# Kernel optimization log

Measured on AMD Instinct MI355X. Metric: run time of the kernel, lower is better.

## Reference

```python
import jax, jax.numpy as jnp
import numpy as np

NEG_SLOPE = 0.2  # PyG GATConv default leaky_relu slope
BN_EPS = 1e-5


def gat_conv(x_src, x_dst, src, dst, w_src, w_dst, att_src, att_dst, bias):
    """Bipartite PyG GATConv, heads=H, concat=False (mean over heads), add_self_loops=True.
    x_src: [Ns, F], x_dst: [Nd, F]; src/dst: [E] int edge index; w_*: [F, H*C]; att_*: [H, C]; bias: [C].
    """
    H, C = att_src.shape
    n_dst = x_dst.shape[0]
    hs = (x_src @ w_src).reshape(-1, H, C)            # [Ns, H, C]
    hd = (x_dst @ w_dst).reshape(-1, H, C)            # [Nd, H, C]
    a_s = (hs * att_src[None]).sum(-1)                # [Ns, H]
    a_d = (hd * att_dst[None]).sum(-1)                # [Nd, H]
    # PyG adds self loops with num_nodes = min(Ns, Nd) for bipartite inputs
    n_loop = min(x_src.shape[0], n_dst)
    loop = jnp.arange(n_loop, dtype=src.dtype)
    src = jnp.concatenate([src, loop])
    dst = jnp.concatenate([dst, loop])
    e = jax.nn.leaky_relu(a_s[src] + a_d[dst], NEG_SLOPE)           # [E+L, H]
    m = jax.ops.segment_max(e, dst, num_segments=n_dst)             # [Nd, H]
    ex = jnp.exp(e - m[dst])
    den = jax.ops.segment_sum(ex, dst, num_segments=n_dst)
    alpha = ex / (den[dst] + 1e-16)                                 # neighborhood softmax
    msg = hs[src] * alpha[:, :, None]                               # [E+L, H, C]
    out = jax.ops.segment_sum(msg, dst, num_segments=n_dst)         # [Nd, H, C]
    return out.mean(axis=1) + bias


def _forward(user_ids, ingredient_ids, recipe_x, ing_src, ing_dst, ub_src, ub_dst,
             user_table, ing_table, W_rl, b_rl, bn_gamma, bn_beta,
             g1_ws, g1_wd, g1_as, g1_ad, g1_b,
             g2_ws, g2_wd, g2_as, g2_ad, g2_b):
    # nn.Embedding(max_norm=1.0): renorm looked-up rows to L2 norm <= 1
    u = user_table[user_ids]
    un = jnp.linalg.norm(u, axis=-1, keepdims=True)
    u = u * jnp.where(un > 1.0, 1.0 / (un + 1e-7), 1.0)
    # static ingredient embedding lookup
    ing = ing_table[ingredient_ids]
    # recipe linear + BatchNorm (training-mode batch stats; dropout off = eval)
    r = recipe_x @ W_rl + b_rl
    mu = r.mean(axis=0)
    var = ((r - mu) ** 2).mean(axis=0)
    r = bn_gamma * (r - mu) * jax.lax.rsqrt(var + BN_EPS) + bn_beta
    # ingredient -> recipe GAT, residual add
    r = r + gat_conv(ing, r, ing_src, ing_dst, g1_ws, g1_wd, g1_as, g1_ad, g1_b)
    # user -> recipe GAT
    r = gat_conv(u, r, ub_src, ub_dst, g2_ws, g2_wd, g2_as, g2_ad, g2_b)
    return r


def setup_inputs() -> dict:
    key = jax.random.key(0)
    ks = jax.random.split(key, 24)
    NU, NR, NI = 50000, 100000, 20000
    D_IN, H, C = 20, 2, 128
    E1, E2 = 400000, 800000
    s = 0.05
    f32 = jnp.float32
    inp = {
        "user_ids": jax.random.randint(ks[0], (NU,), 0, NU, dtype=jnp.int32),
        "ingredient_ids": jax.random.randint(ks[1], (NI,), 0, NI, dtype=jnp.int32),
        "recipe_x": jax.random.normal(ks[2], (NR, D_IN), f32),
        "ing_src": jax.random.randint(ks[3], (E1,), 0, NI, dtype=jnp.int32),
        "ing_dst": jax.random.randint(ks[4], (E1,), 0, NR, dtype=jnp.int32),
        "ub_src": jax.random.randint(ks[5], (E2,), 0, NU, dtype=jnp.int32),
        "ub_dst": jax.random.randint(ks[6], (E2,), 0, NR, dtype=jnp.int32),
        "user_table": jax.random.normal(ks[7], (NU, C), f32) * s,
        "ing_table": jax.random.normal(ks[8], (NI, C), f32) * s,
        "W_rl": jax.random.normal(ks[9], (D_IN, C), f32) * s,
        "b_rl": jnp.zeros((C,), f32),
        "bn_gamma": jnp.ones((C,), f32),
        "bn_beta": jnp.zeros((C,), f32),
        "g1_ws": jax.random.normal(ks[10], (C, H * C), f32) * s,
        "g1_wd": jax.random.normal(ks[11], (C, H * C), f32) * s,
        "g1_as": jax.random.normal(ks[12], (H, C), f32) * s,
        "g1_ad": jax.random.normal(ks[13], (H, C), f32) * s,
        "g1_b": jnp.zeros((C,), f32),
        "g2_ws": jax.random.normal(ks[14], (C, H * C), f32) * s,
        "g2_wd": jax.random.normal(ks[15], (C, H * C), f32) * s,
        "g2_as": jax.random.normal(ks[16], (H, C), f32) * s,
        "g2_ad": jax.random.normal(ks[17], (H, C), f32) * s,
        "g2_b": jnp.zeros((C,), f32),
    }
    return inp


def reference(user_ids, ingredient_ids, recipe_x, ing_src, ing_dst, ub_src, ub_dst,
              user_table, ing_table, W_rl, b_rl, bn_gamma, bn_beta,
              g1_ws, g1_wd, g1_as, g1_ad, g1_b,
              g2_ws, g2_wd, g2_as, g2_ad, g2_b):
    return _forward(user_ids, ingredient_ids, recipe_x, ing_src, ing_dst, ub_src, ub_dst,
                    user_table, ing_table, W_rl, b_rl, bn_gamma, bn_beta,
                    g1_ws, g1_wd, g1_as, g1_ad, g1_b,
                    g2_ws, g2_wd, g2_as, g2_ad, g2_b)
```

## Files before the change

### kernel.cpp

```cpp
#include <hip/hip_runtime.h>
#include <hip/hip_bf16.h>
#include <math.h>

#define DIN 20
#define C 128
#define HC 256
#define EB1 8192
#define EB2 2048
#define MAXNB 400

typedef unsigned short u16;
typedef unsigned int u32;
typedef unsigned long long u64;
typedef __bf16 bf16x8 __attribute__((ext_vector_type(8)));
typedef float f32x4 __attribute__((ext_vector_type(4)));

__device__ __forceinline__ float bfbits2f(unsigned int lo16) {
    return __uint_as_float(lo16 << 16);
}
__device__ __forceinline__ u16 f2bf_rne(float f) {
    unsigned int b = __float_as_uint(f);
    return (u16)((b + 0x7FFFu + ((b >> 16) & 1u)) >> 16);
}

__device__ __forceinline__ void scan512f(u32* cnt, u32* off, u32* wsum4) {
    int t = threadIdx.x;
    int l = t & 63, w = t >> 6;
    u32 a = cnt[2 * t], b = cnt[2 * t + 1];
    u32 s = a + b;
    u32 isc = s;
    #pragma unroll
    for (int o = 1; o < 64; o <<= 1) {
        u32 n = __shfl_up(isc, o);
        if (l >= o) isc += n;
    }
    if (l == 63) wsum4[w] = isc;
    __syncthreads();
    u32 pre = 0;
    if (w > 0) pre += wsum4[0];
    if (w > 1) pre += wsum4[1];
    if (w > 2) pre += wsum4[2];
    u32 excl = pre + isc - s;
    off[2 * t] = excl;
    off[2 * t + 1] = excl + a;
    __syncthreads();
}

__device__ __forceinline__ void edge_at(int i, const int* s1, const int* d1,
    const int* s2, const int* d2, int E1, int T1, int E2, int NR,
    int& s, int& key)
{
    if (i < T1) {
        if (i < E1) { s = s1[i]; key = d1[i]; }
        else        { s = i - E1; key = i - E1; }
    } else {
        int k = i - T1;
        if (k < E2) { s = s2[k]; key = NR + d2[k]; }
        else        { s = k - E2; key = NR + (k - E2); }
    }
}

__global__ __launch_bounds__(256) void k_init(const float* __restrict__ x, int NR,
    float* __restrict__ stats, int SB,
    const int* __restrict__ src1, const int* __restrict__ dst1,
    const int* __restrict__ src2, const int* __restrict__ dst2,
    int E1, int L1, int E2, int L2, int NB, u32* __restrict__ bucketCnt)
{
    __shared__ float L[256][DIN];
    __shared__ u32 cnt[MAXNB];
    int t = threadIdx.x;
    if (blockIdx.x < SB) {
        int r = blockIdx.x * 256 + t;
        if (r < NR) {
            #pragma unroll
            for (int k = 0; k < DIN; k++) L[t][k] = x[r * DIN + k];
        } else {
            #pragma unroll
            for (int k = 0; k < DIN; k++) L[t][k] = 0.f;
        }
        __syncthreads();
        if (t < 210) {
            int p = 0, q = t;
            while (q >= DIN - p) { q -= (DIN - p); p++; }
            q += p;
            float acc = 0.f;
            for (int rr = 0; rr < 256; rr++) acc += L[rr][p] * L[rr][q];
            atomicAdd(&stats[p * DIN + q], acc);
            if (p != q) atomicAdd(&stats[q * DIN + p], acc);
        } else if (t < 230) {
            int k = t - 210;
            float acc = 0.f;
            for (int rr = 0; rr < 256; rr++) acc += L[rr][k];
            atomicAdd(&stats[400 + k], acc);
        }
        return;
    }
    for (int i = t; i < NB; i += 256) cnt[i] = 0;
    __syncthreads();
    int T1 = E1 + L1, T = T1 + E2 + L2;
    int base = (blockIdx.x - SB) * EB1;
    int nE = T - base; if (nE > EB1) nE = EB1;
    for (int j = t; j < nE; j += 256) {
        int s, key;
        edge_at(base + j, src1, dst1, src2, dst2, E1, T1, E2, NR, s, key);
        atomicAdd(&cnt[key >> 9], 1u);
    }
    __syncthreads();
    for (int b = t; b < NB; b += 256) {
        u32 c = cnt[b];
        if (c) atomicAdd(&bucketCnt[b], c);
    }
}

__global__ __launch_bounds__(256) void k_precomp_pack(float* __restrict__ stats,
    const float* __restrict__ W,
    const float* __restrict__ gamma, const float* __restrict__ beta,
    const float* __restrict__ g1_wd, const float* __restrict__ g1_ad,
    const float* __restrict__ g2_wd, const float* __restrict__ g2_ad,
    const float* __restrict__ g1_ws, const float* __restrict__ g1_as,
    const float* __restrict__ g2_ws, const float* __restrict__ g2_as,
    const float* __restrict__ g1b, float invN, u16* __restrict__ wsp,
    const u32* __restrict__ bucketCnt, int NB, int n2,
    u32* __restrict__ bucketBase, u32* __restrict__ gcur, int* __restrict__ off)
{
    int t = threadIdx.x;
    if (blockIdx.x == 33) {
        __shared__ u32 cnt[512], offL[512], wsum4[4];
        for (int i = t; i < 512; i += 256) cnt[i] = (i < NB) ? bucketCnt[i] : 0u;
        __syncthreads();
        scan512f(cnt, offL, wsum4);
        for (int i = t; i < NB; i += 256) {
            u32 v = offL[i];
            bucketBase[i] = v;
            gcur[i] = v;
        }
        if (t == 0) {
            u32 total = offL[511] + cnt[511];
            bucketBase[NB] = total;
            off[n2] = (int)total;
        }
        return;
    }
    if (blockIdx.x > 0) {
        int idx0 = ((blockIdx.x - 1) * 256 + t) * 4;
        #pragma unroll
        for (int i = 0; i < 4; i++) {
            int flat = idx0 + i;
            int j = flat & 7;
            int lane = (flat >> 3) & 63;
            int kb = (flat >> 9) & 3;
            int nt = flat >> 11;
            int k = kb * 32 + (lane >> 4) * 8 + j;
            int n = nt * 16 + (lane & 15);
            wsp[flat] = f2bf_rne(g2_ws[k * HC + n]);
        }
        return;
    }
    __shared__ float Sm[420];
    __shared__ float Wm[DIN * C];
    __shared__ float vd1s[256];
    __shared__ float vd2s[256];
    __shared__ float sS[128];
    __shared__ float sSh[128];
    for (int i = t; i < 420; i += 256) Sm[i] = stats[i];
    for (int i = t; i < DIN * C; i += 256) Wm[i] = W[i];
    __syncthreads();
    if (t < C) {
        float w[DIN];
        #pragma unroll
        for (int k = 0; k < DIN; k++) w[k] = Wm[k * C + t];
        float mb = 0.f;
        #pragma unroll
        for (int k = 0; k < DIN; k++) mb += Sm[400 + k] * invN * w[k];
        float e2 = 0.f;
        for (int p = 0; p < DIN; p++) {
            float acc2 = 0.f;
            #pragma unroll
            for (int q = 0; q < DIN; q++) acc2 += Sm[p * DIN + q] * w[q];
            e2 += w[p] * acc2;
        }
        e2 *= invN;
        float var = e2 - mb * mb;
        float s = gamma[t] * rsqrtf(var + 1e-5f);
        float sh = beta[t] - s * mb;
        stats[420 + t] = s;
        stats[548 + t] = sh;
        sS[t] = s;
        sSh[t] = sh;
    }
    {
        int k = t >> 1, h = t & 1;
        const float4* wd1 = (const float4*)(g1_wd + k * HC + h * C);
        const float4* wd2 = (const float4*)(g2_wd + k * HC + h * C);
        const float4* ws1 = (const float4*)(g1_ws + k * HC + h * C);
        const float4* ws2 = (const float4*)(g2_ws + k * HC + h * C);
        const float4* ad1 = (const float4*)(g1_ad + h * C);
        const float4* ad2 = (const float4*)(g2_ad + h * C);
        const float4* as1 = (const float4*)(g1_as + h * C);
        const float4* as2 = (const float4*)(g2_as + h * C);
        float a1 = 0.f, a2 = 0.f, s1 = 0.f, s2 = 0.f;
        #pragma unroll 4
        for (int q = 0; q < 32; q++) {
            float4 x, y;
            x = wd1[q]; y = ad1[q];
            a1 += x.x * y.x + x.y * y.y + x.z * y.z + x.w * y.w;
            x = wd2[q]; y = ad2[q];
            a2 += x.x * y.x + x.y * y.y + x.z * y.z + x.w * y.w;
            x = ws1[q]; y = as1[q];
            s1 += x.x * y.x + x.y * y.y + x.z * y.z + x.w * y.w;
            x = ws2[q]; y = as2[q];
            s2 += x.x * y.x + x.y * y.y + x.z * y.z + x.w * y.w;
        }
        stats[676 + t] = a1;
        stats[932 + t] = a2;
        stats[1200 + t] = s1;
        stats[1456 + t] = s2;
        vd1s[t] = a1;
        vd2s[t] = a2;
    }
    __syncthreads();
    {
        int k = t >> 1, h = t & 1;
        const float4* ws1p = (const float4*)(g1_ws + k * HC + h * C);
        float t0 = 0.f, t1 = 0.f;
        #pragma unroll 4
        for (int q = 0; q < 32; q++) {
            float4 wv = ws1p[q];
            int c = q * 4;
            t0 += wv.x * vd2s[(c + 0) * 2 + 0] + wv.y * vd2s[(c + 1) * 2 + 0]
                + wv.z * vd2s[(c + 2) * 2 + 0] + wv.w * vd2s[(c + 3) * 2 + 0];
            t1 += wv.x * vd2s[(c + 0) * 2 + 1] + wv.y * vd2s[(c + 1) * 2 + 1]
                + wv.z * vd2s[(c + 2) * 2 + 1] + wv.w * vd2s[(c + 3) * 2 + 1];
        }
        stats[1712 + t * 2 + 0] = t0;
        stats[1712 + t * 2 + 1] = t1;
    }
    if (t < 2) {
        float cb = 0.f;
        for (int k = 0; k < C; k++) cb += g1b[k] * vd2s[k * 2 + t];
        stats[1188 + t] = cb;
    }
    if (t < 80) {
        int k = t >> 2, h4 = t & 3, h = h4 & 1;
        const float* vs = (h4 < 2) ? vd1s : vd2s;
        float acc = 0.f;
        for (int c = 0; c < C; c++) acc += sS[c] * Wm[k * C + c] * vs[c * 2 + h];
        stats[2240 + t] = acc;
    } else if (t < 84) {
        int h4 = t - 80, h = h4 & 1;
        const float* vs = (h4 < 2) ? vd1s : vd2s;
        float acc = 0.f;
        for (int c = 0; c < C; c++) acc += sSh[c] * vs[c * 2 + h];
        stats[2320 + h4] = acc;
    }
}

__global__ __launch_bounds__(256) void k_feat(
    const float* __restrict__ x, int NR, int R0B, int IB,
    const float* __restrict__ ing_table, const int* __restrict__ ing_ids, int NI,
    const float* __restrict__ user_table, const int* __restrict__ user_ids, int NU,
    const u16* __restrict__ wsp, const float* __restrict__ stats,
    float* __restrict__ a_d, float* __restrict__ advd,
    float* __restrict__ a_si, float* __restrict__ psi,
    u16* __restrict__ hs16, float* __restrict__ a_su)
{
    __shared__ float fv[84];
    __shared__ float u1s[256];
    __shared__ float Ts[512];
    __shared__ __align__(16) u16 A[32 * 136];
    __shared__ float u2s[256];
    int t = threadIdx.x;
    int bid = blockIdx.x;
    if (bid < R0B) {
        if (t < 84) fv[t] = stats[2240 + t];
        __syncthreads();
        int r = bid * 256 + t;
        if (r < NR) {
            const float4* xp = (const float4*)(x + (size_t)r * DIN);
            float4 v0 = xp[0], v1 = xp[1], v2 = xp[2], v3 = xp[3], v4 = xp[4];
            float xv[20] = {v0.x, v0.y, v0.z, v0.w, v1.x, v1.y, v1.z, v1.w,
                            v2.x, v2.y, v2.z, v2.w, v3.x, v3.y, v3.z, v3.w,
                            v4.x, v4.y, v4.z, v4.w};
            float a0 = 0.f, a1 = 0.f, b0 = 0.f, b1 = 0.f;
            #pragma unroll
            for (int k = 0; k < DIN; k++) {
                float xvk = xv[k];
                a0 += xvk * fv[k * 4 + 0];
                a1 += xvk * fv[k * 4 + 1];
                b0 += xvk * fv[k * 4 + 2];
                b1 += xvk * fv[k * 4 + 3];
            }
            ((float2*)a_d)[r]  = make_float2(a0 + fv[80], a1 + fv[81]);
            ((float2*)advd)[r] = make_float2(b0 + fv[82], b1 + fv[83]);
        }
        return;
    }
    if (bid < R0B + IB) {
        u1s[t] = stats[1200 + t];
        Ts[t] = stats[1712 + t];
        Ts[256 + t] = stats[1968 + t];
        __syncthreads();
        int r = t >> 3, cg = t & 7;
        int row = (bid - R0B) * 32 + r;
        float as0 = 0.f, as1 = 0.f, p00 = 0.f, p01 = 0.f, p10 = 0.f, p11 = 0.f;
        if (row < NI) {
            const float* xp = ing_table + (size_t)ing_ids[row] * C + cg * 16;
            #pragma unroll
            for (int q = 0; q < 4; q++) {
                float4 v = ((const float4*)xp)[q];
                float xvv[4] = {v.x, v.y, v.z, v.w};
                #pragma unroll
                for (int jj = 0; jj < 4; jj++) {
                    int k = cg * 16 + q * 4 + jj;
                    float xx = xvv[jj];
                    as0 += xx * u1s[k * 2 + 0];
                    as1 += xx * u1s[k * 2 + 1];
                    p00 += xx * Ts[k * 4 + 0];
                    p01 += xx * Ts[k * 4 + 1];
                    p10 += xx * Ts[k * 4 + 2];
                    p11 += xx * Ts[k * 4 + 3];
                }
            }
        }
        #pragma unroll
        for (int m = 1; m <= 4; m <<= 1) {
            as0 += __shfl_xor(as0, m); as1 += __shfl_xor(as1, m);
            p00 += __shfl_xor(p00, m); p01 += __shfl_xor(p01, m);
            p10 += __shfl_xor(p10, m); p11 += __shfl_xor(p11, m);
        }
        if (cg == 0 && row < NI) {
            ((float2*)a_si)[row] = make_float2(as0, as1);
            float4 pv; pv.x = p00; pv.y = p01; pv.z = p10; pv.w = p11;
            ((float4*)psi)[row] = pv;
        }
        return;
    }
    u2s[t] = stats[1456 + t];
    int rowBase = (bid - R0B - IB) * 32;
    int r = t >> 3, cg = t & 7;
    int row = rowBase + r;
    float xv[16];
    if (row < NU) {
        const float* xp = user_table + (size_t)user_ids[row] * C + cg * 16;
        #pragma unroll
        for (int q = 0; q < 4; q++) {
            float4 v = ((const float4*)xp)[q];
            xv[q * 4 + 0] = v.x; xv[q * 4 + 1] = v.y;
            xv[q * 4 + 2] = v.z; xv[q * 4 + 3] = v.w;
        }
    } else {
        #pragma unroll
        for (int q = 0; q < 16; q++) xv[q] = 0.f;
    }
    float ss = 0.f;
    #pragma unroll
    for (int q = 0; q < 16; q++) ss += xv[q] * xv[q];
    #pragma unroll
    for (int m = 1; m <= 4; m <<= 1) ss += __shfl_xor(ss, m);
    float nn = sqrtf(ss);
    float f = (nn > 1.f) ? 1.f / (nn + 1e-7f) : 1.f;
    float as0 = 0.f, as1 = 0.f;
    #pragma unroll
    for (int q = 0; q < 16; q++) {
        xv[q] *= f;
        int k = cg * 16 + q;
        as0 += xv[q] * u2s[k * 2 + 0];
        as1 += xv[q] * u2s[k * 2 + 1];
    }
    #pragma unroll
    for (int m = 1; m <= 4; m <<= 1) {
        as0 += __shfl_xor(as0, m); as1 += __shfl_xor(as1, m);
    }
    if (cg == 0 && row < NU) ((float2*)a_su)[row] = make_float2(as0, as1);
    {
        union { u16 h[16]; uint4 u4[2]; } pk;
        #pragma unroll
        for (int q = 0; q < 16; q++) pk.h[q] = f2bf_rne(xv[q]);
        uint4* dst = (uint4*)&A[r * 136 + cg * 16];
        dst[0] = pk.u4[0];
        dst[1] = pk.u4[1];
    }
    __syncthreads();
    int w = t >> 6, l = t & 63;
    int m15 = l & 15, q4 = l >> 4;
    bf16x8 afrag[2][4];
    #pragma unroll
    for (int mt = 0; mt < 2; mt++)
        #pragma unroll
        for (int kb = 0; kb < 4; kb++)
            afrag[mt][kb] = *(const bf16x8*)&A[(mt * 16 + m15) * 136 + kb * 32 + q4 * 8];
    f32x4 acc[2][4];
    #pragma unroll
    for (int mt = 0; mt < 2; mt++)
        #pragma unroll
        for (int i = 0; i < 4; i++) acc[mt][i] = (f32x4){0.f, 0.f, 0.f, 0.f};
    #pragma unroll
    for (int kb = 0; kb < 4; kb++) {
        #pragma unroll
        for (int i = 0; i < 4; i++) {
            int nt = w * 4 + i;
            bf16x8 bfrag = *(const bf16x8*)&wsp[((nt * 4 + kb) * 64 + l) * 8];
            acc[0][i] = __builtin_amdgcn_mfma_f32_16x16x32_bf16(afrag[0][kb], bfrag, acc[0][i], 0, 0, 0);
            acc[1][i] = __builtin_amdgcn_mfma_f32_16x16x32_bf16(afrag[1][kb], bfrag, acc[1][i], 0, 0, 0);
        }
    }
    #pragma unroll
    for (int mt = 0; mt < 2; mt++) {
        #pragma unroll
        for (int i = 0; i < 4; i++) {
            int col = (w * 4 + i) * 16 + m15;
            #pragma unroll
            for (int rr = 0; rr < 4; rr++) {
                int rw = rowBase + mt * 16 + q4 * 4 + rr;
                if (rw < NU) hs16[(size_t)rw * HC + col] = f2bf_rne(acc[mt][i][rr]);
            }
        }
    }
}

__global__ __launch_bounds__(256) void kA2(const int* __restrict__ src1, const int* __restrict__ dst1,
    const int* __restrict__ src2, const int* __restrict__ dst2,
    int E1, int L1, int E2, int L2, int NR, int NB,
    u32* __restrict__ gcur, u64* __restrict__ pairs)
{
    __shared__ u64 ldsE[EB2];
    __shared__ u64 ldsS[EB2];
    __shared__ u32 cntA[512], cntB[512], offL[512], wsum4[4];
    __shared__ u32 gbase[MAXNB];
    int t = threadIdx.x;
    for (int i = t; i < 512; i += 256) { cntA[i] = 0; cntB[i] = 0; }
    __syncthreads();
    int T1 = E1 + L1, T = T1 + E2 + L2;
    int base = blockIdx.x * EB2;
    int nE = T - base; if (nE > EB2) nE = EB2;
    for (int j = t; j < nE; j += 256) {
        int s, key;
        edge_at(base + j, src1, dst1, src2, dst2, E1, T1, E2, NR, s, key);
        ldsE[j] = ((u64)(u32)key << 32) | (u32)s;
        atomicAdd(&cntA[key >> 9], 1u);
    }
    __syncthreads();
    scan512f(cntA, offL, wsum4);
    for (int b = t; b < NB; b += 256) {
        u32 c = cntA[b];
        gbase[b] = c ? atomicAdd(&gcur[b], c) : 0u;
    }
    __syncthreads();
    for (int j = t; j < nE; j += 256) {
        u64 e = ldsE[j];
        u32 b = ((u32)(e >> 32)) >> 9;
        u32 r = atomicAdd(&cntB[b], 1u);
        ldsS[offL[b] + r] = e;
    }
    __syncthreads();
    for (int j = t; j < nE; j += 256) {
        u64 e = ldsS[j];
        u32 b = ((u32)(e >> 32)) >> 9;
        pairs[gbase[b] + ((u32)j - offL[b])] = e;
    }
}

__global__ __launch_bounds__(256) void kB(const u64* __restrict__ pairs,
    const u32* __restrict__ bucketBase, int n2,
    int* __restrict__ off, int* __restrict__ sorted)
{
    __shared__ u32 cntA[512], cntB[512], offL[512], wsum4[4];
    __shared__ u32 ldsS[8192];
    int b = blockIdx.x;
    int t = threadIdx.x;
    u32 beg = bucketBase[b], end = bucketBase[b + 1];
    int dstBase = b << 9;
    for (int i = t; i < 512; i += 256) { cntA[i] = 0; cntB[i] = 0; }
    __syncthreads();
    for (u32 j = beg + t; j < end; j += 256) {
        u32 key = (u32)(pairs[j] >> 32);
        atomicAdd(&cntA[key - dstBase], 1u);
    }
    __syncthreads();
    scan512f(cntA, offL, wsum4);
    for (int d = t; d < 512; d += 256) {
        int gk = dstBase + d;
        if (gk < n2) off[gk] = (int)(beg + offL[d]);
    }
    u32 cnt = end - beg;
    bool fast = cnt <= 8192u;
    __syncthreads();
    for (u32 j = beg + t; j < end; j += 256) {
        u64 e = pairs[j];
        u32 d = (u32)(e >> 32) - dstBase;
        u32 r = atomicAdd(&cntB[d], 1u);
        u32 pos = offL[d] + r;
        if (fast) ldsS[pos] = (u32)e;
        else sorted[beg + pos] = (int)(u32)e;
    }
    __syncthreads();
    if (fast) {
        for (u32 j = t; j < cnt; j += 256) sorted[beg + j] = (int)ldsS[j];
    }
}

__global__ __launch_bounds__(256) void k_agg(const int* __restrict__ off, const int* __restrict__ sorted,
    const float* __restrict__ a_si, const float* __restrict__ psi,
    const float* __restrict__ a_d1, const float* __restrict__ advd,
    const float* __restrict__ cb,
    const float* __restrict__ a_su, const u16* __restrict__ hs16,
    const float* __restrict__ bias, int NR, float* __restrict__ out)
{
    int wave = threadIdx.x >> 6, lane = threadIdx.x & 63;
    int d = blockIdx.x * 4 + wave;
    if (d >= NR) return;
    int beg = off[d], end = off[d + 1];
    float ad0 = a_d1[d * 2 + 0], ad1 = a_d1[d * 2 + 1];
    float w0s = 0.f, w1s = 0.f, a00 = 0.f, a01 = 0.f, a10 = 0.f, a11 = 0.f;
    for (int j = beg + lane; j < end; j += 64) {
        int s = sorted[j];
        float2 as = ((const float2*)a_si)[s];
        float e0 = as.x + ad0; e0 = (e0 >= 0.f) ? e0 : 0.2f * e0;
        float e1 = as.y + ad1; e1 = (e1 >= 0.f) ? e1 : 0.2f * e1;
        float x0 = __expf(e0), x1 = __expf(e1);
        float4 p = ((const float4*)psi)[s];
        w0s += x0; w1s += x1;
        a00 += x0 * p.x; a01 += x0 * p.y;
        a10 += x1 * p.z; a11 += x1 * p.w;
    }
    #pragma unroll
    for (int o = 1; o < 64; o <<= 1) {
        w0s += __shfl_xor(w0s, o); w1s += __shfl_xor(w1s, o);
        a00 += __shfl_xor(a00, o); a01 += __shfl_xor(a01, o);
        a10 += __shfl_xor(a10, o); a11 += __shfl_xor(a11, o);
    }
    float inv0g = 1.f / (w0s + 1e-16f), inv1g = 1.f / (w1s + 1e-16f);
    float r0 = advd[d * 2 + 0] + cb[0] + 0.5f * (a00 * inv0g + a10 * inv1g);
    float r1 = advd[d * 2 + 1] + cb[1] + 0.5f * (a01 * inv0g + a11 * inv1g);
    int beg2 = off[NR + d], end2 = off[NR + d + 1];
    int head = lane >> 5;
    int q = lane & 31;
    u32 laneoff = (u32)(head * 256 + q * 8);
    int hsel = lane & 32;
    float adh = head ? r1 : r0;
    float wsum = 0.f;
    float acc0 = 0.f, acc1 = 0.f, acc2 = 0.f, acc3 = 0.f;
    const char* hbase = (const char*)hs16;

    for (int base = beg2; base < end2; base += 32) {
        int rem = end2 - base; if (rem > 32) rem = 32;
        int j = q; if (j >= rem) j = rem - 1;
        int sp = sorted[base + j];
        u32 boff = ((u32)sp) << 9;
        float asv = a_su[sp * 2 + head];
        float ee = asv + adh; ee = (ee >= 0.f) ? ee : 0.2f * ee;
        float wcomb = __expf(ee);
        int e = 0;
        for (; e + 4 <= rem; e += 4) {
            u32 b0 = __shfl(boff, e + 0), b1 = __shfl(boff, e + 1);
            u32 b2 = __shfl(boff, e + 2), b3 = __shfl(boff, e + 3);
            uint2 g0 = *(const uint2*)(hbase + (b0 + laneoff));
            uint2 g1 = *(const uint2*)(hbase + (b1 + laneoff));
            uint2 g2 = *(const uint2*)(hbase + (b2 + laneoff));
            uint2 g3 = *(const uint2*)(hbase + (b3 + laneoff));
            float W0 = __shfl(wcomb, hsel + e + 0);
            float W1 = __shfl(wcomb, hsel + e + 1);
            float W2 = __shfl(wcomb, hsel + e + 2);
            float W3 = __shfl(wcomb, hsel + e + 3);
            wsum += (W0 + W1) + (W2 + W3);
            acc0 += W0 * bfbits2f(g0.x & 0xFFFFu);
            acc1 += W0 * __uint_as_float(g0.x & 0xFFFF0000u);
            acc2 += W0 * bfbits2f(g0.y & 0xFFFFu);
            acc3 += W0 * __uint_as_float(g0.y & 0xFFFF0000u);
            acc0 += W1 * bfbits2f(g1.x & 0xFFFFu);
            acc1 += W1 * __uint_as_float(g1.x & 0xFFFF0000u);
            acc2 += W1 * bfbits2f(g1.y & 0xFFFFu);
            acc3 += W1 * __uint_as_float(g1.y & 0xFFFF0000u);
            acc0 += W2 * bfbits2f(g2.x & 0xFFFFu);
            acc1 += W2 * __uint_as_float(g2.x & 0xFFFF0000u);
            acc2 += W2 * bfbits2f(g2.y & 0xFFFFu);
            acc3 += W2 * __uint_as_float(g2.y & 0xFFFF0000u);
            acc0 += W3 * bfbits2f(g3.x & 0xFFFFu);
            acc1 += W3 * __uint_as_float(g3.x & 0xFFFF0000u);
            acc2 += W3 * bfbits2f(g3.y & 0xFFFFu);
            acc3 += W3 * __uint_as_float(g3.y & 0xFFFF0000u);
        }
        for (; e < rem; e++) {
            u32 b0 = __shfl(boff, e);
            float W = __shfl(wcomb, hsel + e);
            uint2 g = *(const uint2*)(hbase + (b0 + laneoff));
            wsum += W;
            acc0 += W * bfbits2f(g.x & 0xFFFFu);
            acc1 += W * __uint_as_float(g.x & 0xFFFF0000u);
            acc2 += W * bfbits2f(g.y & 0xFFFFu);
            acc3 += W * __uint_as_float(g.y & 0xFFFF0000u);
        }
    }
    float inv = 1.f / (wsum + 1e-16f);
    float v0 = acc0 * inv, v1 = acc1 * inv, v2 = acc2 * inv, v3 = acc3 * inv;
    v0 = 0.5f * (v0 + __shfl_xor(v0, 32));
    v1 = 0.5f * (v1 + __shfl_xor(v1, 32));
    v2 = 0.5f * (v2 + __shfl_xor(v2, 32));
    v3 = 0.5f * (v3 + __shfl_xor(v3, 32));
    if (lane < 32) {
        float4 bb = ((const float4*)bias)[q];
        float4 o;
        o.x = v0 + bb.x; o.y = v1 + bb.y; o.z = v2 + bb.z; o.w = v3 + bb.w;
        ((float4*)(out + (size_t)d * C))[q] = o;
    }
}

extern "C" void kernel_launch(void* const* d_in, const int* in_sizes, int n_in,
                              void* d_out, int out_size, void* d_ws, size_t ws_size,
                              hipStream_t stream) {
    const int*   user_ids       = (const int*)d_in[0];
    const int*   ingredient_ids = (const int*)d_in[1];
    const float* recipe_x       = (const float*)d_in[2];
    const int*   ing_src        = (const int*)d_in[3];
    const int*   ing_dst        = (const int*)d_in[4];
    const int*   ub_src         = (const int*)d_in[5];
    const int*   ub_dst         = (const int*)d_in[6];
    const float* user_table     = (const float*)d_in[7];
    const float* ing_table      = (const float*)d_in[8];
    const float* W_rl           = (const float*)d_in[9];
    const float* bn_gamma       = (const float*)d_in[11];
    const float* bn_beta        = (const float*)d_in[12];
    const float* g1_ws          = (const float*)d_in[13];
    const float* g1_wd          = (const float*)d_in[14];
    const float* g1_as          = (const float*)d_in[15];
    const float* g1_ad          = (const float*)d_in[16];
    const float* g1_b           = (const float*)d_in[17];
    const float* g2_ws          = (const float*)d_in[18];
    const float* g2_wd          = (const float*)d_in[19];
    const float* g2_as          = (const float*)d_in[20];
    const float* g2_ad          = (const float*)d_in[21];
    const float* g2_b           = (const float*)d_in[22];

    int NU = in_sizes[0];
    int NI = in_sizes[1];
    int NR = in_sizes[2] / DIN;
    int E1 = in_sizes[3];
    int E2 = in_sizes[5];
    int Nmax = (NI > NU) ? NI : NU;
    int L1 = (NI < NR) ? NI : NR;
    int L2 = (NU < NR) ? NU : NR;
    int Etot = E1 + L1 + E2 + L2;
    int n2 = 2 * NR;
    int NB = (n2 + 511) >> 9;

    char* w = (char*)d_ws;
    u16*   hs16  = (u16*)w;    w += (size_t)Nmax * HC * 2;
    float* a_si  = (float*)w;  w += (size_t)NI * 2 * 4;
    float* a_su  = (float*)w;  w += (size_t)NU * 2 * 4;
    float* psi   = (float*)w;  w += (size_t)NI * 4 * 4;
    float* a_d   = (float*)w;  w += (size_t)NR * 2 * 4;
    float* advd  = (float*)w;  w += (size_t)NR * 2 * 4;
    float* stats = (float*)w;  w += 2432 * 4;
    u32*   bucketCnt  = (u32*)w; w += MAXNB * 4;
    u16*   wsp   = (u16*)w;    w += 32768 * 2;
    u32*   bucketBase = (u32*)w; w += (MAXNB + 1) * 4;
    u32*   gcur  = (u32*)w;    w += MAXNB * 4;
    int*   off   = (int*)w;    w += (size_t)(n2 + 1) * 4;
    int*   sorted= (int*)w;    w += (size_t)Etot * 4;
    w = (char*)(((size_t)w + 15) & ~(size_t)15);
    u64*   pairs = (u64*)w;    w += (size_t)Etot * 8;

    hipMemsetAsync(stats, 0, (2432 + MAXNB) * 4, stream);

    int SB = (NR + 255) / 256;
    int AB = (Etot + EB1 - 1) / EB1;
    k_init<<<SB + AB, 256, 0, stream>>>(recipe_x, NR, stats, SB,
                                        ing_src, ing_dst, ub_src, ub_dst,
                                        E1, L1, E2, L2, NB, bucketCnt);
    k_precomp_pack<<<34, 256, 0, stream>>>(stats, W_rl, bn_gamma, bn_beta,
                                           g1_wd, g1_ad, g2_wd, g2_ad,
                                           g1_ws, g1_as, g2_ws, g2_as, g1_b,
                                           1.0f / NR, wsp,
                                           bucketCnt, NB, n2, bucketBase, gcur, off);
    kA2<<<(Etot + EB2 - 1) / EB2, 256, 0, stream>>>(ing_src, ing_dst, ub_src, ub_dst,
                                                    E1, L1, E2, L2, NR, NB, gcur, pairs);
    int R0B = (NR + 255) / 256;
    int IB  = (NI + 31) / 32;
    int HB  = (NU + 31) / 32;
    k_feat<<<R0B + IB + HB, 256, 0, stream>>>(recipe_x, NR, R0B, IB,
                                              ing_table, ingredient_ids, NI,
                                              user_table, user_ids, NU,
                                              wsp, stats, a_d, advd, a_si, psi,
                                              hs16, a_su);
    kB<<<NB, 256, 0, stream>>>(pairs, bucketBase, n2, off, sorted);
    k_agg<<<(NR + 3) / 4, 256, 0, stream>>>(off, sorted, a_si, psi, a_d, advd,
                                            stats + 1188, a_su, hs16, g2_b, NR,
                                            (float*)d_out);
}
```

Before: 352.4 us.

## Replace two-pass bucket sort with per-destination counting sort fused into feature kernel

Edge grouping by destination now uses a counting sort: global atomic histogram per destination key, a block-level scan with a tiny second-level prefix, and an atomic scatter of source ids. The scatter runs as extra blocks inside the feature kernel, which removes the kA2 and kB kernels and the 64-bit pairs buffer. The user-aggregation loop also now processes two edges per wave step with 16-byte gathers per lane. The cost is heavy global atomic contention on hot destinations and a non-deterministic order of edges within each segment.

Result: slower. 456.6 us (+29.6%).

```diff
diff --git a/kernel.cpp b/kernel.cpp
--- a/kernel.cpp
+++ b/kernel.cpp
@@ -6,8 +6,7 @@
 #define C 128
 #define HC 256
 #define EB1 8192
-#define EB2 2048
-#define MAXNB 400
+#define EBS 4096
 
 typedef unsigned short u16;
 typedef unsigned int u32;
@@ -23,51 +22,12 @@
     return (u16)((b + 0x7FFFu + ((b >> 16) & 1u)) >> 16);
 }
 
-__device__ __forceinline__ void scan512f(u32* cnt, u32* off, u32* wsum4) {
-    int t = threadIdx.x;
-    int l = t & 63, w = t >> 6;
-    u32 a = cnt[2 * t], b = cnt[2 * t + 1];
-    u32 s = a + b;
-    u32 isc = s;
-    #pragma unroll
-    for (int o = 1; o < 64; o <<= 1) {
-        u32 n = __shfl_up(isc, o);
-        if (l >= o) isc += n;
-    }
-    if (l == 63) wsum4[w] = isc;
-    __syncthreads();
-    u32 pre = 0;
-    if (w > 0) pre += wsum4[0];
-    if (w > 1) pre += wsum4[1];
-    if (w > 2) pre += wsum4[2];
-    u32 excl = pre + isc - s;
-    off[2 * t] = excl;
-    off[2 * t + 1] = excl + a;
-    __syncthreads();
-}
-
-__device__ __forceinline__ void edge_at(int i, const int* s1, const int* d1,
-    const int* s2, const int* d2, int E1, int T1, int E2, int NR,
-    int& s, int& key)
-{
-    if (i < T1) {
-        if (i < E1) { s = s1[i]; key = d1[i]; }
-        else        { s = i - E1; key = i - E1; }
-    } else {
-        int k = i - T1;
-        if (k < E2) { s = s2[k]; key = NR + d2[k]; }
-        else        { s = k - E2; key = NR + (k - E2); }
-    }
-}
-
 __global__ __launch_bounds__(256) void k_init(const float* __restrict__ x, int NR,
     float* __restrict__ stats, int SB,
-    const int* __restrict__ src1, const int* __restrict__ dst1,
-    const int* __restrict__ src2, const int* __restrict__ dst2,
-    int E1, int L1, int E2, int L2, int NB, u32* __restrict__ bucketCnt)
+    const int* __restrict__ dst1, const int* __restrict__ dst2,
+    int E1, int L1, int E2, int L2, u32* __restrict__ gcur)
 {
     __shared__ float L[256][DIN];
-    __shared__ u32 cnt[MAXNB];
     int t = threadIdx.x;
     if (blockIdx.x < SB) {
         int r = blockIdx.x * 256 + t;
@@ -95,21 +55,50 @@
         }
         return;
     }
-    for (int i = t; i < NB; i += 256) cnt[i] = 0;
-    __syncthreads();
     int T1 = E1 + L1, T = T1 + E2 + L2;
     int base = (blockIdx.x - SB) * EB1;
     int nE = T - base; if (nE > EB1) nE = EB1;
     for (int j = t; j < nE; j += 256) {
-        int s, key;
-        edge_at(base + j, src1, dst1, src2, dst2, E1, T1, E2, NR, s, key);
-        atomicAdd(&cnt[key >> 9], 1u);
-    }
+        int i = base + j, key;
+        if (i < T1) key = (i < E1) ? dst1[i] : (i - E1);
+        else { int k = i - T1; key = NR + ((k < E2) ? dst2[k] : (k - E2)); }
+        atomicAdd(&gcur[key], 1u);
+    }
+}
+
+__global__ __launch_bounds__(256) void kScan1(u32* __restrict__ gcur, int n,
+    int* __restrict__ off, u32* __restrict__ partial)
+{
+    __shared__ u32 wsums[4];
+    int t = threadIdx.x;
+    int base = blockIdx.x * 2048 + t * 8;
+    u32 v[8]; u32 s = 0;
+    #pragma unroll
+    for (int i = 0; i < 8; i++) {
+        int gi = base + i;
+        v[i] = (gi < n) ? gcur[gi] : 0u;
+        s += v[i];
+    }
+    int l = t & 63, w = t >> 6;
+    u32 isc = s;
+    #pragma unroll
+    for (int o = 1; o < 64; o <<= 1) {
+        u32 nn = __shfl_up(isc, o);
+        if (l >= o) isc += nn;
+    }
+    if (l == 63) wsums[w] = isc;
     __syncthreads();
-    for (int b = t; b < NB; b += 256) {
-        u32 c = cnt[b];
-        if (c) atomicAdd(&bucketCnt[b], c);
-    }
+    u32 pre = 0;
+    if (w > 0) pre += wsums[0];
+    if (w > 1) pre += wsums[1];
+    if (w > 2) pre += wsums[2];
+    u32 excl = pre + isc - s;
+    #pragma unroll
+    for (int i = 0; i < 8; i++) {
+        int gi = base + i;
+        if (gi < n) { off[gi] = (int)excl; gcur[gi] = 0u; excl += v[i]; }
+    }
+    if (t == 255) partial[blockIdx.x] = pre + isc;
 }
 
 __global__ __launch_bounds__(256) void k_precomp_pack(float* __restrict__ stats,
@@ -120,25 +109,19 @@
     const float* __restrict__ g1_ws, const float* __restrict__ g1_as,
     const float* __restrict__ g2_ws, const float* __restrict__ g2_as,
     const float* __restrict__ g1b, float invN, u16* __restrict__ wsp,
-    const u32* __restrict__ bucketCnt, int NB, int n2,
-    u32* __restrict__ bucketBase, u32* __restrict__ gcur, int* __restrict__ off)
+    const u32* __restrict__ partial, int NPB, u32* __restrict__ pex)
 {
     int t = threadIdx.x;
     if (blockIdx.x == 33) {
-        __shared__ u32 cnt[512], offL[512], wsum4[4];
-        for (int i = t; i < 512; i += 256) cnt[i] = (i < NB) ? bucketCnt[i] : 0u;
+        __shared__ u32 ps[256];
+        ps[t] = (t < NPB) ? partial[t] : 0u;
         __syncthreads();
-        scan512f(cnt, offL, wsum4);
-        for (int i = t; i < NB; i += 256) {
-            u32 v = offL[i];
-            bucketBase[i] = v;
-            gcur[i] = v;
-        }
         if (t == 0) {
-            u32 total = offL[511] + cnt[511];
-            bucketBase[NB] = total;
-            off[n2] = (int)total;
-        }
+            u32 acc = 0;
+            for (int i = 0; i < NPB; i++) { u32 c = ps[i]; ps[i] = acc; acc += c; }
+        }
+        __syncthreads();
+        if (t < NPB) pex[t] = ps[t];
         return;
     }
     if (blockIdx.x > 0) {
@@ -256,13 +239,18 @@
 }
 
 __global__ __launch_bounds__(256) void k_feat(
-    const float* __restrict__ x, int NR, int R0B, int IB,
+    const float* __restrict__ x, int NR, int R0B, int IB, int HB,
     const float* __restrict__ ing_table, const int* __restrict__ ing_ids, int NI,
     const float* __restrict__ user_table, const int* __restrict__ user_ids, int NU,
     const u16* __restrict__ wsp, const float* __restrict__ stats,
     float* __restrict__ a_d, float* __restrict__ advd,
     float* __restrict__ a_si, float* __restrict__ psi,
-    u16* __restrict__ hs16, float* __restrict__ a_su)
+    u16* __restrict__ hs16, float* __restrict__ a_su,
+    const int* __restrict__ src1, const int* __restrict__ dst1,
+    const int* __restrict__ src2, const int* __restrict__ dst2,
+    int E1, int L1, int E2, int L2,
+    const int* __restrict__ off, const u32* __restrict__ pex,
+    u32* __restrict__ gcur, int* __restrict__ sorted)
 {
     __shared__ float fv[84];
     __shared__ float u1s[256];
@@ -335,171 +323,111 @@
         }
         return;
     }
-    u2s[t] = stats[1456 + t];
-    int rowBase = (bid - R0B - IB) * 32;
-    int r = t >> 3, cg = t & 7;
-    int row = rowBase + r;
-    float xv[16];
-    if (row < NU) {
-        const float* xp = user_table + (size_t)user_ids[row] * C + cg * 16;
-        #pragma unroll
-        for (int q = 0; q < 4; q++) {
-            float4 v = ((const float4*)xp)[q];
-            xv[q * 4 + 0] = v.x; xv[q * 4 + 1] = v.y;
-            xv[q * 4 + 2] = v.z; xv[q * 4 + 3] = v.w;
-        }
-    } else {
-        #pragma unroll
-        for (int q = 0; q < 16; q++) xv[q] = 0.f;
-    }
-    float ss = 0.f;
-    #pragma unroll
-    for (int q = 0; q < 16; q++) ss += xv[q] * xv[q];
-    #pragma unroll
-    for (int m = 1; m <= 4; m <<= 1) ss += __shfl_xor(ss, m);
-    float nn = sqrtf(ss);
-    float f = (nn > 1.f) ? 1.f / (nn + 1e-7f) : 1.f;
-    float as0 = 0.f, as1 = 0.f;
-    #pragma unroll
-    for (int q = 0; q < 16; q++) {
-        xv[q] *= f;
-        int k = cg * 16 + q;
-        as0 += xv[q] * u2s[k * 2 + 0];
-        as1 += xv[q] * u2s[k * 2 + 1];
-    }
-    #pragma unroll
-    for (int m = 1; m <= 4; m <<= 1) {
-        as0 += __shfl_xor(as0, m); as1 += __shfl_xor(as1, m);
-    }
-    if (cg == 0 && row < NU) ((float2*)a_su)[row] = make_float2(as0, as1);
-    {
-        union { u16 h[16]; uint4 u4[2]; } pk;
-        #pragma unroll
-        for (int q = 0; q < 16; q++) pk.h[q] = f2bf_rne(xv[q]);
-        uint4* dst = (uint4*)&A[r * 136 + cg * 16];
-        dst[0] = pk.u4[0];
-        dst[1] = pk.u4[1];
-    }
-    __syncthreads();
-    int w = t >> 6, l = t & 63;
-    int m15 = l & 15, q4 = l >> 4;
-    bf16x8 afrag[2][4];
-    #pragma unroll
-    for (int mt = 0; mt < 2; mt++)
-        #pragma unroll
-        for (int kb = 0; kb < 4; kb++)
-            afrag[mt][kb] = *(const bf16x8*)&A[(mt * 16 + m15) * 136 + kb * 32 + q4 * 8];
-    f32x4 acc[2][4];
-    #pragma unroll
-    for (int mt = 0; mt < 2; mt++)
-        #pragma unroll
-        for (int i = 0; i < 4; i++) acc[mt][i] = (f32x4){0.f, 0.f, 0.f, 0.f};
-    #pragma unroll
-    for (int kb = 0; kb < 4; kb++) {
-        #pragma unroll
-        for (int i = 0; i < 4; i++) {
-            int nt = w * 4 + i;
-            bf16x8 bfrag = *(const bf16x8*)&wsp[((nt * 4 + kb) * 64 + l) * 8];
-            acc[0][i] = __builtin_amdgcn_mfma_f32_16x16x32_bf16(afrag[0][kb], bfrag, acc[0][i], 0, 0, 0);
-            acc[1][i] = __builtin_amdgcn_mfma_f32_16x16x32_bf16(afrag[1][kb], bfrag, acc[1][i], 0, 0, 0);
-        }
-    }
-    #pragma unroll
-    for (int mt = 0; mt < 2; mt++) {
-        #pragma unroll
-        for (int i = 0; i < 4; i++) {
-            int col = (w * 4 + i) * 16 + m15;
-            #pragma unroll
-            for (int rr = 0; rr < 4; rr++) {
-                int rw = rowBase + mt * 16 + q4 * 4 + rr;
-                if (rw < NU) hs16[(size_t)rw * HC + col] = f2bf_rne(acc[mt][i][rr]);
+    if (bid < R0B + IB + HB) {
+        u2s[t] = stats[1456 + t];
+        int rowBase = (bid - R0B - IB) * 32;
+        int r = t >> 3, cg = t & 7;
+        int row = rowBase + r;
+        float xv[16];
+        if (row < NU) {
+            const float* xp = user_table + (size_t)user_ids[row] * C + cg * 16;
+            #pragma unroll
+            for (int q = 0; q < 4; q++) {
+                float4 v = ((const float4*)xp)[q];
+                xv[q * 4 + 0] = v.x; xv[q * 4 + 1] = v.y;
+                xv[q * 4 + 2] = v.z; xv[q * 4 + 3] = v.w;
             }
-        }
-    }
-}
-
-__global__ __launch_bounds__(256) void kA2(const int* __restrict__ src1, const int* __restrict__ dst1,
-    const int* __restrict__ src2, const int* __restrict__ dst2,
-    int E1, int L1, int E2, int L2, int NR, int NB,
-    u32* __restrict__ gcur, u64* __restrict__ pairs)
-{
-    __shared__ u64 ldsE[EB2];
-    __shared__ u64 ldsS[EB2];
-    __shared__ u32 cntA[512], cntB[512], offL[512], wsum4[4];
-    __shared__ u32 gbase[MAXNB];
-    int t = threadIdx.x;
-    for (int i = t; i < 512; i += 256) { cntA[i] = 0; cntB[i] = 0; }
-    __syncthreads();
+        } else {
+            #pragma unroll
+            for (int q = 0; q < 16; q++) xv[q] = 0.f;
+        }
+        float ss = 0.f;
+        #pragma unroll
+        for (int q = 0; q < 16; q++) ss += xv[q] * xv[q];
+        #pragma unroll
+        for (int m = 1; m <= 4; m <<= 1) ss += __shfl_xor(ss, m);
+        float nn = sqrtf(ss);
+        float f = (nn > 1.f) ? 1.f / (nn + 1e-7f) : 1.f;
+        float as0 = 0.f, as1 = 0.f;
+        #pragma unroll
+        for (int q = 0; q < 16; q++) {
+            xv[q] *= f;
+            int k = cg * 16 + q;
+            as0 += xv[q] * u2s[k * 2 + 0];
+            as1 += xv[q] * u2s[k * 2 + 1];
+        }
+        #pragma unroll
+        for (int m = 1; m <= 4; m <<= 1) {
+            as0 += __shfl_xor(as0, m); as1 += __shfl_xor(as1, m);
+        }
+        if (cg == 0 && row < NU) ((float2*)a_su)[row] = make_float2(as0, as1);
+        {
+            union { u16 h[16]; uint4 u4[2]; } pk;
+            #pragma unroll
+            for (int q = 0; q < 16; q++) pk.h[q] = f2bf_rne(xv[q]);
+            uint4* dst = (uint4*)&A[r * 136 + cg * 16];
+            dst[0] = pk.u4[0];
+            dst[1] = pk.u4[1];
+        }
+        __syncthreads();
+        int w = t >> 6, l = t & 63;
+        int m15 = l & 15, q4 = l >> 4;
+        bf16x8 afrag[2][4];
+        #pragma unroll
+        for (int mt = 0; mt < 2; mt++)
+            #pragma unroll
+            for (int kb = 0; kb < 4; kb++)
+                afrag[mt][kb] = *(const bf16x8*)&A[(mt * 16 + m15) * 136 + kb * 32 + q4 * 8];
+        f32x4 acc[2][4];
+        #pragma unroll
+        for (int mt = 0; mt < 2; mt++)
+            #pragma unroll
+            for (int i = 0; i < 4; i++) acc[mt][i] = (f32x4){0.f, 0.f, 0.f, 0.f};
+        #pragma unroll
+        for (int kb = 0; kb < 4; kb++) {
+            #pragma unroll
+            for (int i = 0; i < 4; i++) {
+                int nt = w * 4 + i;
+                bf16x8 bfrag = *(const bf16x8*)&wsp[((nt * 4 + kb) * 64 + l) * 8];
+                acc[0][i] = __builtin_amdgcn_mfma_f32_16x16x32_bf16(afrag[0][kb], bfrag, acc[0][i], 0, 0, 0);
+                acc[1][i] = __builtin_amdgcn_mfma_f32_16x16x32_bf16(afrag[1][kb], bfrag, acc[1][i], 0, 0, 0);
+            }
+        }
+        #pragma unroll
+        for (int mt = 0; mt < 2; mt++) {
+            #pragma unroll
+            for (int i = 0; i < 4; i++) {
+                int col = (w * 4 + i) * 16 + m15;
+                #pragma unroll
+                for (int rr = 0; rr < 4; rr++) {
+                    int rw = rowBase + mt * 16 + q4 * 4 + rr;
+                    if (rw < NU) hs16[(size_t)rw * HC + col] = f2bf_rne(acc[mt][i][rr]);
+                }
+            }
+        }
+        return;
+    }
+    int sb = bid - R0B - IB - HB;
     int T1 = E1 + L1, T = T1 + E2 + L2;
-    int base = blockIdx.x * EB2;
-    int nE = T - base; if (nE > EB2) nE = EB2;
+    int base = sb * EBS;
+    int nE = T - base; if (nE > EBS) nE = EBS;
     for (int j = t; j < nE; j += 256) {
-        int s, key;
-        edge_at(base + j, src1, dst1, src2, dst2, E1, T1, E2, NR, s, key);
-        ldsE[j] = ((u64)(u32)key << 32) | (u32)s;
-        atomicAdd(&cntA[key >> 9], 1u);
-    }
-    __syncthreads();
-    scan512f(cntA, offL, wsum4);
-    for (int b = t; b < NB; b += 256) {
-        u32 c = cntA[b];
-        gbase[b] = c ? atomicAdd(&gcur[b], c) : 0u;
-    }
-    __syncthreads();
-    for (int j = t; j < nE; j += 256) {
-        u64 e = ldsE[j];
-        u32 b = ((u32)(e >> 32)) >> 9;
-        u32 r = atomicAdd(&cntB[b], 1u);
-        ldsS[offL[b] + r] = e;
-    }
-    __syncthreads();
-    for (int j = t; j < nE; j += 256) {
-        u64 e = ldsS[j];
-        u32 b = ((u32)(e >> 32)) >> 9;
-        pairs[gbase[b] + ((u32)j - offL[b])] = e;
-    }
-}
-
-__global__ __launch_bounds__(256) void kB(const u64* __restrict__ pairs,
-    const u32* __restrict__ bucketBase, int n2,
-    int* __restrict__ off, int* __restrict__ sorted)
-{
-    __shared__ u32 cntA[512], cntB[512], offL[512], wsum4[4];
-    __shared__ u32 ldsS[8192];
-    int b = blockIdx.x;
-    int t = threadIdx.x;
-    u32 beg = bucketBase[b], end = bucketBase[b + 1];
-    int dstBase = b << 9;
-    for (int i = t; i < 512; i += 256) { cntA[i] = 0; cntB[i] = 0; }
-    __syncthreads();
-    for (u32 j = beg + t; j < end; j += 256) {
-        u32 key = (u32)(pairs[j] >> 32);
-        atomicAdd(&cntA[key - dstBase], 1u);
-    }
-    __syncthreads();
-    scan512f(cntA, offL, wsum4);
-    for (int d = t; d < 512; d += 256) {
-        int gk = dstBase + d;
-        if (gk < n2) off[gk] = (int)(beg + offL[d]);
-    }
-    u32 cnt = end - beg;
-    bool fast = cnt <= 8192u;
-    __syncthreads();
-    for (u32 j = beg + t; j < end; j += 256) {
-        u64 e = pairs[j];
-        u32 d = (u32)(e >> 32) - dstBase;
-        u32 r = atomicAdd(&cntB[d], 1u);
-        u32 pos = offL[d] + r;
-        if (fast) ldsS[pos] = (u32)e;
-        else sorted[beg + pos] = (int)(u32)e;
-    }
-    __syncthreads();
-    if (fast) {
-        for (u32 j = t; j < cnt; j += 256) sorted[beg + j] = (int)ldsS[j];
-    }
-}
-
-__global__ __launch_bounds__(256) void k_agg(const int* __restrict__ off, const int* __restrict__ sorted,
+        int i = base + j, s, key;
+        if (i < T1) {
+            if (i < E1) { s = src1[i]; key = dst1[i]; }
+            else        { s = i - E1; key = i - E1; }
+        } else {
+            int k = i - T1;
+            if (k < E2) { s = src2[k]; key = NR + dst2[k]; }
+            else        { s = k - E2; key = NR + (k - E2); }
+        }
+        u32 pos = (u32)off[key] + pex[key >> 11] + atomicAdd(&gcur[key], 1u);
+        sorted[pos] = s;
+    }
+}
+
+__global__ __launch_bounds__(256) void k_agg(const int* __restrict__ off,
+    const u32* __restrict__ pex, const int* __restrict__ sorted,
     const float* __restrict__ a_si, const float* __restrict__ psi,
     const float* __restrict__ a_d1, const float* __restrict__ advd,
     const float* __restrict__ cb,
@@ -509,7 +437,8 @@
     int wave = threadIdx.x >> 6, lane = threadIdx.x & 63;
     int d = blockIdx.x * 4 + wave;
     if (d >= NR) return;
-    int beg = off[d], end = off[d + 1];
+    int beg = off[d] + (int)pex[d >> 11];
+    int end = off[d + 1] + (int)pex[(d + 1) >> 11];
     float ad0 = a_d1[d * 2 + 0], ad1 = a_d1[d * 2 + 1];
     float w0s = 0.f, w1s = 0.f, a00 = 0.f, a01 = 0.f, a10 = 0.f, a11 = 0.f;
     for (int j = beg + lane; j < end; j += 64) {
@@ -532,76 +461,67 @@
     float inv0g = 1.f / (w0s + 1e-16f), inv1g = 1.f / (w1s + 1e-16f);
     float r0 = advd[d * 2 + 0] + cb[0] + 0.5f * (a00 * inv0g + a10 * inv1g);
     float r1 = advd[d * 2 + 1] + cb[1] + 0.5f * (a01 * inv0g + a11 * inv1g);
-    int beg2 = off[NR + d], end2 = off[NR + d + 1];
-    int head = lane >> 5;
-    int q = lane & 31;
-    u32 laneoff = (u32)(head * 256 + q * 8);
-    int hsel = lane & 32;
-    float adh = head ? r1 : r0;
+    int i2 = NR + d;
+    int beg2 = off[i2] + (int)pex[i2 >> 11];
+    int end2 = off[i2 + 1] + (int)pex[(i2 + 1) >> 11];
+    int g = lane >> 5;
+    int lg = lane & 31;
+    int head = lg >> 4;
+    int hq = lg & 15;
+    u32 laneoff = (u32)(head * 256 + hq * 16);
+    int hsel = head << 5;
+    float adh = (lane >= 32) ? r1 : r0;
     float wsum = 0.f;
-    float acc0 = 0.f, acc1 = 0.f, acc2 = 0.f, acc3 = 0.f;
+    float acc[8];
+    #pragma unroll
+    for (int k = 0; k < 8; k++) acc[k] = 0.f;
     const char* hbase = (const char*)hs16;
 
     for (int base = beg2; base < end2; base += 32) {
         int rem = end2 - base; if (rem > 32) rem = 32;
-        int j = q; if (j >= rem) j = rem - 1;
+        int j = lg; if (j >= rem) j = rem - 1;
         int sp = sorted[base + j];
         u32 boff = ((u32)sp) << 9;
-        float asv = a_su[sp * 2 + head];
+        float asv = a_su[sp * 2 + g];
         float ee = asv + adh; ee = (ee >= 0.f) ? ee : 0.2f * ee;
         float wcomb = __expf(ee);
-        int e = 0;
-        for (; e + 4 <= rem; e += 4) {
-            u32 b0 = __shfl(boff, e + 0), b1 = __shfl(boff, e + 1);
-            u32 b2 = __shfl(boff, e + 2), b3 = __shfl(boff, e + 3);
-            uint2 g0 = *(const uint2*)(hbase + (b0 + laneoff));
-            uint2 g1 = *(const uint2*)(hbase + (b1 + laneoff));
-            uint2 g2 = *(const uint2*)(hbase + (b2 + laneoff));
-            uint2 g3 = *(const uint2*)(hbase + (b3 + laneoff));
-            float W0 = __shfl(wcomb, hsel + e + 0);
-            float W1 = __shfl(wcomb, hsel + e + 1);
-            float W2 = __shfl(wcomb, hsel + e + 2);
-            float W3 = __shfl(wcomb, hsel + e + 3);
-            wsum += (W0 + W1) + (W2 + W3);
-            acc0 += W0 * bfbits2f(g0.x & 0xFFFFu);
-            acc1 += W0 * __uint_as_float(g0.x & 0xFFFF0000u);
-            acc2 += W0 * bfbits2f(g0.y & 0xFFFFu);
-            acc3 += W0 * __uint_as_float(g0.y & 0xFFFF0000u);
-            acc0 += W1 * bfbits2f(g1.x & 0xFFFFu);
-            acc1 += W1 * __uint_as_float(g1.x & 0xFFFF0000u);
-            acc2 += W1 * bfbits2f(g1.y & 0xFFFFu);
-            acc3 += W1 * __uint_as_float(g1.y & 0xFFFF0000u);
-            acc0 += W2 * bfbits2f(g2.x & 0xFFFFu);
-            acc1 += W2 * __uint_as_float(g2.x & 0xFFFF0000u);
-            acc2 += W2 * bfbits2f(g2.y & 0xFFFFu);
-            acc3 += W2 * __uint_as_float(g2.y & 0xFFFF0000u);
-            acc0 += W3 * bfbits2f(g3.x & 0xFFFFu);
-            acc1 += W3 * __uint_as_float(g3.x & 0xFFFF0000u);
-            acc2 += W3 * bfbits2f(g3.y & 0xFFFFu);
-            acc3 += W3 * __uint_as_float(g3.y & 0xFFFF0000u);
-        }
-        for (; e < rem; e++) {
-            u32 b0 = __shfl(boff, e);
-            float W = __shfl(wcomb, hsel + e);
-            uint2 g = *(const uint2*)(hbase + (b0 + laneoff));
+        for (int e = 0; e < rem; e += 2) {
+            int eg = e + g;
+            bool valid = eg < rem;
+            int srcl = valid ? eg : rem - 1;
+            u32 bo = __shfl(boff, srcl);
+            float W = __shfl(wcomb, hsel + srcl);
+            W = valid ? W : 0.f;
+            uint4 gg = *(const uint4*)(hbase + (bo + laneoff));
             wsum += W;
-            acc0 += W * bfbits2f(g.x & 0xFFFFu);
-            acc1 += W * __uint_as_float(g.x & 0xFFFF0000u);
-            acc2 += W * bfbits2f(g.y & 0xFFFFu);
-            acc3 += W * __uint_as_float(g.y & 0xFFFF0000u);
-        }
-    }
+            acc[0] += W * bfbits2f(gg.x & 0xFFFFu);
+            acc[1] += W * __uint_as_float(gg.x & 0xFFFF0000u);
+            acc[2] += W * bfbits2f(gg.y & 0xFFFFu);
+            acc[3] += W * __uint_as_float(gg.y & 0xFFFF0000u);
+            acc[4] += W * bfbits2f(gg.z & 0xFFFFu);
+            acc[5] += W * __uint_as_float(gg.z & 0xFFFF0000u);
+            acc[6] += W * bfbits2f(gg.w & 0xFFFFu);
+            acc[7] += W * __uint_as_float(gg.w & 0xFFFF0000u);
+        }
+    }
+    wsum += __shfl_xor(wsum, 32);
+    #pragma unroll
+    for (int k = 0; k < 8; k++) acc[k] += __shfl_xor(acc[k], 32);
     float inv = 1.f / (wsum + 1e-16f);
-    float v0 = acc0 * inv, v1 = acc1 * inv, v2 = acc2 * inv, v3 = acc3 * inv;
-    v0 = 0.5f * (v0 + __shfl_xor(v0, 32));
-    v1 = 0.5f * (v1 + __shfl_xor(v1, 32));
-    v2 = 0.5f * (v2 + __shfl_xor(v2, 32));
-    v3 = 0.5f * (v3 + __shfl_xor(v3, 32));
-    if (lane < 32) {
-        float4 bb = ((const float4*)bias)[q];
-        float4 o;
-        o.x = v0 + bb.x; o.y = v1 + bb.y; o.z = v2 + bb.z; o.w = v3 + bb.w;
-        ((float4*)(out + (size_t)d * C))[q] = o;
+    #pragma unroll
+    for (int k = 0; k < 8; k++) acc[k] *= inv;
+    #pragma unroll
+    for (int k = 0; k < 8; k++) acc[k] = 0.5f * (acc[k] + __shfl_xor(acc[k], 16));
+    if (lane < 16) {
+        const float4* b4 = (const float4*)bias;
+        float4 bb0 = b4[hq * 2], bb1 = b4[hq * 2 + 1];
+        float4 o0, o1;
+        o0.x = acc[0] + bb0.x; o0.y = acc[1] + bb0.y;
+        o0.z = acc[2] + bb0.z; o0.w = acc[3] + bb0.w;
+        o1.x = acc[4] + bb1.x; o1.y = acc[5] + bb1.y;
+        o1.z = acc[6] + bb1.z; o1.w = acc[7] + bb1.w;
+        float4* op = (float4*)(out + (size_t)d * C + hq * 8);
+        op[0] = o0; op[1] = o1;
     }
 }
 
@@ -641,7 +561,7 @@
     int L2 = (NU < NR) ? NU : NR;
     int Etot = E1 + L1 + E2 + L2;
     int n2 = 2 * NR;
-    int NB = (n2 + 511) >> 9;
+    int NPB = (n2 + 1 + 2047) >> 11;
 
     char* w = (char*)d_ws;
     u16*   hs16  = (u16*)w;    w += (size_t)Nmax * HC * 2;
@@ -651,39 +571,36 @@
     float* a_d   = (float*)w;  w += (size_t)NR * 2 * 4;
     float* advd  = (float*)w;  w += (size_t)NR * 2 * 4;
     float* stats = (float*)w;  w += 2432 * 4;
-    u32*   bucketCnt  = (u32*)w; w += MAXNB * 4;
+    u32*   gcur  = (u32*)w;    w += (size_t)(n2 + 1) * 4;
     u16*   wsp   = (u16*)w;    w += 32768 * 2;
-    u32*   bucketBase = (u32*)w; w += (MAXNB + 1) * 4;
-    u32*   gcur  = (u32*)w;    w += MAXNB * 4;
     int*   off   = (int*)w;    w += (size_t)(n2 + 1) * 4;
+    u32*   partial = (u32*)w;  w += 256 * 4;
+    u32*   pex   = (u32*)w;    w += 256 * 4;
     int*   sorted= (int*)w;    w += (size_t)Etot * 4;
-    w = (char*)(((size_t)w + 15) & ~(size_t)15);
-    u64*   pairs = (u64*)w;    w += (size_t)Etot * 8;
-
-    hipMemsetAsync(stats, 0, (2432 + MAXNB) * 4, stream);
+
+    hipMemsetAsync(stats, 0, (size_t)(2432 + n2 + 1) * 4, stream);
 
     int SB = (NR + 255) / 256;
     int AB = (Etot + EB1 - 1) / EB1;
     k_init<<<SB + AB, 256, 0, stream>>>(recipe_x, NR, stats, SB,
-                                        ing_src, ing_dst, ub_src, ub_dst,
-                                        E1, L1, E2, L2, NB, bucketCnt);
+                                        ing_dst, ub_dst, E1, L1, E2, L2, gcur);
+    kScan1<<<NPB, 256, 0, stream>>>(gcur, n2 + 1, off, partial);
     k_precomp_pack<<<34, 256, 0, stream>>>(stats, W_rl, bn_gamma, bn_beta,
                                            g1_wd, g1_ad, g2_wd, g2_ad,
                                            g1_ws, g1_as, g2_ws, g2_as, g1_b,
-                                           1.0f / NR, wsp,
-                                           bucketCnt, NB, n2, bucketBase, gcur, off);
-    kA2<<<(Etot + EB2 - 1) / EB2, 256, 0, stream>>>(ing_src, ing_dst, ub_src, ub_dst,
-                                                    E1, L1, E2, L2, NR, NB, gcur, pairs);
+                                           1.0f / NR, wsp, partial, NPB, pex);
     int R0B = (NR + 255) / 256;
     int IB  = (NI + 31) / 32;
     int HB  = (NU + 31) / 32;
-    k_feat<<<R0B + IB + HB, 256, 0, stream>>>(recipe_x, NR, R0B, IB,
+    int SCB = (Etot + EBS - 1) / EBS;
+    k_feat<<<R0B + IB + HB + SCB, 256, 0, stream>>>(recipe_x, NR, R0B, IB, HB,
                                               ing_table, ingredient_ids, NI,
                                               user_table, user_ids, NU,
                                               wsp, stats, a_d, advd, a_si, psi,
-                                              hs16, a_su);
-    kB<<<NB, 256, 0, stream>>>(pairs, bucketBase, n2, off, sorted);
-    k_agg<<<(NR + 3) / 4, 256, 0, stream>>>(off, sorted, a_si, psi, a_d, advd,
+                                              hs16, a_su,
+                                              ing_src, ing_dst, ub_src, ub_dst,
+                                              E1, L1, E2, L2, off, pex, gcur, sorted);
+    k_agg<<<(NR + 3) / 4, 256, 0, stream>>>(off, pex, sorted, a_si, psi, a_d, advd,
                                             stats + 1188, a_su, hs16, g2_b, NR,
                                             (float*)d_out);
 }
```
